# Kernel tuning notes

Measured on AMD Instinct MI355X. Metric: run time of the kernel, lower is better.

Reference implementation:

```python
import jax, jax.numpy as jnp
import numpy as np

EPS = 1e-06
SIGMA_C = 2.0


def setup_inputs() -> dict:
    key = jax.random.key(0)
    k1, k2 = jax.random.split(key)
    B, L, D, T = 16, 512, 256, 2048
    text = jax.random.normal(k1, (B, L, D), dtype=jnp.float32)
    durs = jax.random.randint(k2, (B, L), 0, 8, dtype=jnp.int64)
    return {"text": text, "durs": durs, "total_time": T}


def reference(text, durs, total_time):
    # text: [B, L, D], durs: [B, L] int, total_time: static python int T
    d = durs.astype(jnp.float32)
    # NOTE: faithful to original: mean = durs/2 + cumsum(durs) (cumsum includes current dur)
    mean = d / 2.0 + jnp.cumsum(d, axis=-1)            # [B, L]
    sigma = d / SIGMA_C + EPS                          # [B, L]
    t = jnp.arange(total_time, dtype=jnp.float32) + 0.5  # [T]
    # Normal pdf evaluated at t: exp(log_prob) = exp(-0.5 z^2) / (sigma * sqrt(2 pi))
    z = (t[None, :, None] - mean[:, None, :]) / sigma[:, None, :]  # [B, T, L]
    inv_norm = 1.0 / (sigma[:, None, :] * jnp.sqrt(2.0 * jnp.pi))
    probs = jnp.exp(-0.5 * z * z) * inv_norm           # [B, T, L]
    probs = probs / (probs.sum(-1, keepdims=True) + EPS)
    return jnp.einsum("btl,bld->btd", probs, text)     # [B, T, D]
```

## Files before the change

### kernel.cpp

```cpp
#include <hip/hip_runtime.h>
#include <math.h>

#define L 512
#define LPAD 544
#define NTHREADS 256
#define BLOCK_TT 32
#define ZWIN 9.0f
#define NXCD 8

typedef __attribute__((ext_vector_type(8))) short bf16x8;
typedef __attribute__((ext_vector_type(4))) float f32x4;

static constexpr float EPS = 1e-6f;
static constexpr float INV_SQRT_2PI = 0.39894228040143267794f;

union BFrag { unsigned int u[4]; bf16x8 h; };

__global__ __launch_bounds__(NTHREADS, 4) void ge_mfma(
    const int*   __restrict__ durs,
    const float* __restrict__ text,
    float*       __restrict__ out,
    int B, int T, int tilesPerB, int nwg)
{
    __shared__ float2 s_mi[LPAD];

    const int tid  = threadIdx.x;
    const int lane = tid & 63;
    const int wid  = tid >> 6;
    const int g    = lane >> 4;
    const int mrow = lane & 15;

    const int orig = blockIdx.x;
    const int wg   = (nwg % NXCD == 0) ? (orig & (NXCD - 1)) * (nwg / NXCD) + (orig >> 3)
                                       : orig;
    const int b      = wg / tilesPerB;
    const int tbase0 = (wg % tilesPerB) * BLOCK_TT;

    const int r0 = lane << 3;
    const int4 da = ((const int4*)(durs + (size_t)b * L + r0))[0];
    const int4 db = ((const int4*)(durs + (size_t)b * L + r0))[1];
    int dv[8] = {da.x, da.y, da.z, da.w, db.x, db.y, db.z, db.w};
    int cs[8];
    int run = 0;
    #pragma unroll
    for (int j = 0; j < 8; ++j) { run += dv[j]; cs[j] = run; }
    int v = run;
    #pragma unroll
    for (int off = 1; off < 64; off <<= 1) {
        int n = __shfl_up(v, off, 64);
        if (lane >= off) v += n;
    }
    const int excl = v - run;

    const float tlo = (float)tbase0 + 0.5f;
    const float thi = (float)tbase0 + (float)BLOCK_TT - 0.5f;
    int mn = L, mx = -1;
    #pragma unroll
    for (int j = 0; j < 8; ++j) {
        const float d  = (float)dv[j];
        const float m  = (float)(cs[j] + excl) + 0.5f * d;
        const float sg = 0.5f * d + EPS;
        s_mi[r0 + j] = make_float2(m, 1.0f / sg);
        const float r = ZWIN * sg;
        if (dv[j] >= 1 && m + r >= tlo && m - r <= thi) {
            mn = min(mn, r0 + j);
            mx = max(mx, r0 + j);
        }
    }
    if (lane < LPAD - L) s_mi[L + lane] = make_float2(0.f, 0.f);
    #pragma unroll
    for (int off = 32; off > 0; off >>= 1) {
        mn = min(mn, __shfl_xor(mn, off, 64));
        mx = max(mx, __shfl_xor(mx, off, 64));
    }
    asm volatile("s_waitcnt lgkmcnt(0)" ::: "memory");
    __builtin_amdgcn_sched_barrier(0);

    f32x4 a00 = {0,0,0,0}, a01 = {0,0,0,0}, a02 = {0,0,0,0}, a03 = {0,0,0,0};
    f32x4 a10 = {0,0,0,0}, a11 = {0,0,0,0}, a12 = {0,0,0,0}, a13 = {0,0,0,0};
    float psum0 = 0.f, psum1 = 0.f;
    const float tf0 = (float)(tbase0 + mrow) + 0.5f;
    const float tf1 = tf0 + 16.f;
    const float* tbp = text + (size_t)b * L * 256 + (wid << 6) + mrow;

    for (int kb = (mn & ~7); kb <= mx; kb += 32) {
        const int k0 = kb + (g << 3);

        BFrag B0, B1, B2, B3;
        #pragma unroll
        for (int jp = 0; jp < 4; ++jp) {
            const int ka = min(k0 + 2 * jp,     L - 1);
            const int kc = min(k0 + 2 * jp + 1, L - 1);
            const float* ra = tbp + (size_t)ka * 256;
            const float* rc = tbp + (size_t)kc * 256;
            const float b0 = ra[0], b1 = ra[16], b2 = ra[32], b3 = ra[48];
            const float c0 = rc[0], c1 = rc[16], c2 = rc[32], c3 = rc[48];
            asm("v_cvt_pk_bf16_f32 %0, %1, %2" : "=v"(B0.u[jp]) : "v"(b0), "v"(c0));
            asm("v_cvt_pk_bf16_f32 %0, %1, %2" : "=v"(B1.u[jp]) : "v"(b1), "v"(c1));
            asm("v_cvt_pk_bf16_f32 %0, %1, %2" : "=v"(B2.u[jp]) : "v"(b2), "v"(c2));
            asm("v_cvt_pk_bf16_f32 %0, %1, %2" : "=v"(B3.u[jp]) : "v"(b3), "v"(c3));
        }

        BFrag A0, A1;
        #pragma unroll
        for (int jp = 0; jp < 4; ++jp) {
            const int ka = k0 + 2 * jp;
            const int kc = ka + 1;
            const float2 mia = s_mi[ka];
            const float2 mic = s_mi[kc];
            const float ca = mia.y * INV_SQRT_2PI;
            const float cc = mic.y * INV_SQRT_2PI;
            const float u0a = (tf0 - mia.x) * mia.y;
            const float u0c = (tf0 - mic.x) * mic.y;
            const float u1a = (tf1 - mia.x) * mia.y;
            const float u1c = (tf1 - mic.x) * mic.y;
            const float p0a = __expf(-0.5f * u0a * u0a) * ca;
            const float p0c = __expf(-0.5f * u0c * u0c) * cc;
            const float p1a = __expf(-0.5f * u1a * u1a) * ca;
            const float p1c = __expf(-0.5f * u1c * u1c) * cc;
            psum0 += p0a + p0c;
            psum1 += p1a + p1c;
            asm("v_cvt_pk_bf16_f32 %0, %1, %2" : "=v"(A0.u[jp]) : "v"(p0a), "v"(p0c));
            asm("v_cvt_pk_bf16_f32 %0, %1, %2" : "=v"(A1.u[jp]) : "v"(p1a), "v"(p1c));
        }

        a00 = __builtin_amdgcn_mfma_f32_16x16x32_bf16(A0.h, B0.h, a00, 0, 0, 0);
        a01 = __builtin_amdgcn_mfma_f32_16x16x32_bf16(A0.h, B1.h, a01, 0, 0, 0);
        a02 = __builtin_amdgcn_mfma_f32_16x16x32_bf16(A0.h, B2.h, a02, 0, 0, 0);
        a03 = __builtin_amdgcn_mfma_f32_16x16x32_bf16(A0.h, B3.h, a03, 0, 0, 0);
        a10 = __builtin_amdgcn_mfma_f32_16x16x32_bf16(A1.h, B0.h, a10, 0, 0, 0);
        a11 = __builtin_amdgcn_mfma_f32_16x16x32_bf16(A1.h, B1.h, a11, 0, 0, 0);
        a12 = __builtin_amdgcn_mfma_f32_16x16x32_bf16(A1.h, B2.h, a12, 0, 0, 0);
        a13 = __builtin_amdgcn_mfma_f32_16x16x32_bf16(A1.h, B3.h, a13, 0, 0, 0);
    }

    const int trow = g << 2;
    #pragma unroll
    for (int half = 0; half < 2; ++half) {
        float ps = half ? psum1 : psum0;
        ps += __shfl_xor(ps, 16, 64);
        ps += __shfl_xor(ps, 32, 64);
        const float rn = 1.0f / (ps + EPS);

        const float rr0 = __shfl(rn, trow + 0, 64);
        const float rr1 = __shfl(rn, trow + 1, 64);
        const float rr2 = __shfl(rn, trow + 2, 64);
        const float rr3 = __shfl(rn, trow + 3, 64);

        const f32x4 c0 = half ? a10 : a00;
        const f32x4 c1 = half ? a11 : a01;
        const f32x4 c2 = half ? a12 : a02;
        const f32x4 c3 = half ? a13 : a03;

        const int t0 = tbase0 + (half << 4);
        float* ob = out + ((size_t)b * T + t0 + trow) * 256 + (wid << 6) + mrow;
        if (t0 + trow + 3 < T) {
            __builtin_nontemporal_store(c0[0] * rr0, ob + 0*256 +  0);
            __builtin_nontemporal_store(c0[1] * rr1, ob + 1*256 +  0);
            __builtin_nontemporal_store(c0[2] * rr2, ob + 2*256 +  0);
            __builtin_nontemporal_store(c0[3] * rr3, ob + 3*256 +  0);
            __builtin_nontemporal_store(c1[0] * rr0, ob + 0*256 + 16);
            __builtin_nontemporal_store(c1[1] * rr1, ob + 1*256 + 16);
            __builtin_nontemporal_store(c1[2] * rr2, ob + 2*256 + 16);
            __builtin_nontemporal_store(c1[3] * rr3, ob + 3*256 + 16);
            __builtin_nontemporal_store(c2[0] * rr0, ob + 0*256 + 32);
            __builtin_nontemporal_store(c2[1] * rr1, ob + 1*256 + 32);
            __builtin_nontemporal_store(c2[2] * rr2, ob + 2*256 + 32);
            __builtin_nontemporal_store(c2[3] * rr3, ob + 3*256 + 32);
            __builtin_nontemporal_store(c3[0] * rr0, ob + 0*256 + 48);
            __builtin_nontemporal_store(c3[1] * rr1, ob + 1*256 + 48);
            __builtin_nontemporal_store(c3[2] * rr2, ob + 2*256 + 48);
            __builtin_nontemporal_store(c3[3] * rr3, ob + 3*256 + 48);
        }
    }
}

extern "C" void kernel_launch(void* const* d_in, const int* in_sizes, int n_in,
                              void* d_out, int out_size, void* d_ws, size_t ws_size,
                              hipStream_t stream) {
    const int*   durs = (const int*)d_in[1];
    const float* text = (const float*)d_in[0];
    float*       out  = (float*)d_out;

    const int BL = in_sizes[1];
    const int D  = in_sizes[0] / BL;
    const int B  = BL / L;
    const int T  = out_size / (B * D);
    const int tilesPerB = (T + BLOCK_TT - 1) / BLOCK_TT;
    const int nwg = B * tilesPerB;

    ge_mfma<<<dim3(nwg), dim3(NTHREADS), 0, stream>>>(durs, text, out, B, T, tilesPerB, nwg);
}
```

Before: 14.57 us.

## Compute Gaussian weights once per block in LDS instead of per wave

Each of the four waves previously recomputed the same 32x32 tile of Gaussian probabilities. Now only waves 0 and 1 compute them, each handling one 16-row half, and write bf16 fragments and row sums to shared memory, which all waves read before the MFMAs. This removes redundant exp work but adds a __syncthreads per k-step, LDS traffic, and leaves two waves idle during the weight computation. Row sums are accumulated in shared memory and read in the epilogue, and a double-buffered fragment index is used.

```diff
diff --git a/kernel.cpp b/kernel.cpp
--- a/kernel.cpp
+++ b/kernel.cpp
@@ -14,7 +14,7 @@
 static constexpr float EPS = 1e-6f;
 static constexpr float INV_SQRT_2PI = 0.39894228040143267794f;
 
-union BFrag { unsigned int u[4]; bf16x8 h; };
+union BFrag { unsigned int u[4]; uint4 q; bf16x8 h; };
 
 __global__ __launch_bounds__(NTHREADS, 4) void ge_mfma(
     const int*   __restrict__ durs,
@@ -23,6 +23,8 @@
     int B, int T, int tilesPerB, int nwg)
 {
     __shared__ float2 s_mi[LPAD];
+    __shared__ uint4  s_af[2][2][64];
+    __shared__ float  s_ps[2][16];
 
     const int tid  = threadIdx.x;
     const int lane = tid & 63;
@@ -67,21 +69,19 @@
             mx = max(mx, r0 + j);
         }
     }
-    if (lane < LPAD - L) s_mi[L + lane] = make_float2(0.f, 0.f);
+    if (tid < LPAD - L) s_mi[L + tid] = make_float2(0.f, 0.f);
+    if (tid < 32) s_ps[tid >> 4][tid & 15] = 0.f;
     #pragma unroll
     for (int off = 32; off > 0; off >>= 1) {
         mn = min(mn, __shfl_xor(mn, off, 64));
         mx = max(mx, __shfl_xor(mx, off, 64));
     }
-    asm volatile("s_waitcnt lgkmcnt(0)" ::: "memory");
-    __builtin_amdgcn_sched_barrier(0);
+    __syncthreads();
 
     f32x4 a00 = {0,0,0,0}, a01 = {0,0,0,0}, a02 = {0,0,0,0}, a03 = {0,0,0,0};
     f32x4 a10 = {0,0,0,0}, a11 = {0,0,0,0}, a12 = {0,0,0,0}, a13 = {0,0,0,0};
-    float psum0 = 0.f, psum1 = 0.f;
-    const float tf0 = (float)(tbase0 + mrow) + 0.5f;
-    const float tf1 = tf0 + 16.f;
     const float* tbp = text + (size_t)b * L * 256 + (wid << 6) + mrow;
+    int p = 0;
 
     for (int kb = (mn & ~7); kb <= mx; kb += 32) {
         const int k0 = kb + (g << 3);
@@ -101,28 +101,48 @@
             asm("v_cvt_pk_bf16_f32 %0, %1, %2" : "=v"(B3.u[jp]) : "v"(b3), "v"(c3));
         }
 
+        if (wid < 2) {
+            const float tf = (float)(tbase0 + (wid << 4) + mrow) + 0.5f;
+            float part = 0.f;
+            unsigned int u0, u1, u2, u3;
+            {
+                const float2 mia = s_mi[k0 + 0], mic = s_mi[k0 + 1];
+                const float pa = __expf(-0.5f * ((tf - mia.x) * mia.y) * ((tf - mia.x) * mia.y)) * mia.y * INV_SQRT_2PI;
+                const float pc = __expf(-0.5f * ((tf - mic.x) * mic.y) * ((tf - mic.x) * mic.y)) * mic.y * INV_SQRT_2PI;
+                part += pa + pc;
+                asm("v_cvt_pk_bf16_f32 %0, %1, %2" : "=v"(u0) : "v"(pa), "v"(pc));
+            }
+            {
+                const float2 mia = s_mi[k0 + 2], mic = s_mi[k0 + 3];
+                const float pa = __expf(-0.5f * ((tf - mia.x) * mia.y) * ((tf - mia.x) * mia.y)) * mia.y * INV_SQRT_2PI;
+                const float pc = __expf(-0.5f * ((tf - mic.x) * mic.y) * ((tf - mic.x) * mic.y)) * mic.y * INV_SQRT_2PI;
+                part += pa + pc;
+                asm("v_cvt_pk_bf16_f32 %0, %1, %2" : "=v"(u1) : "v"(pa), "v"(pc));
+            }
+            {
+                const float2 mia = s_mi[k0 + 4], mic = s_mi[k0 + 5];
+                const float pa = __expf(-0.5f * ((tf - mia.x) * mia.y) * ((tf - mia.x) * mia.y)) * mia.y * INV_SQRT_2PI;
+                const float pc = __expf(-0.5f * ((tf - mic.x) * mic.y) * ((tf - mic.x) * mic.y)) * mic.y * INV_SQRT_2PI;
+                part += pa + pc;
+                asm("v_cvt_pk_bf16_f32 %0, %1, %2" : "=v"(u2) : "v"(pa), "v"(pc));
+            }
+            {
+                const float2 mia = s_mi[k0 + 6], mic = s_mi[k0 + 7];
+                const float pa = __expf(-0.5f * ((tf - mia.x) * mia.y) * ((tf - mia.x) * mia.y)) * mia.y * INV_SQRT_2PI;
+                const float pc = __expf(-0.5f * ((tf - mic.x) * mic.y) * ((tf - mic.x) * mic.y)) * mic.y * INV_SQRT_2PI;
+                part += pa + pc;
+                asm("v_cvt_pk_bf16_f32 %0, %1, %2" : "=v"(u3) : "v"(pa), "v"(pc));
+            }
+            part += __shfl_xor(part, 16, 64);
+            part += __shfl_xor(part, 32, 64);
+            if (lane < 16) s_ps[wid][lane] += part;
+            s_af[p][wid][lane] = make_uint4(u0, u1, u2, u3);
+        }
+        __syncthreads();
+
         BFrag A0, A1;
-        #pragma unroll
-        for (int jp = 0; jp < 4; ++jp) {
-            const int ka = k0 + 2 * jp;
-            const int kc = ka + 1;
-            const float2 mia = s_mi[ka];
-            const float2 mic = s_mi[kc];
-            const float ca = mia.y * INV_SQRT_2PI;
-            const float cc = mic.y * INV_SQRT_2PI;
-            const float u0a = (tf0 - mia.x) * mia.y;
-            const float u0c = (tf0 - mic.x) * mic.y;
-            const float u1a = (tf1 - mia.x) * mia.y;
-            const float u1c = (tf1 - mic.x) * mic.y;
-            const float p0a = __expf(-0.5f * u0a * u0a) * ca;
-            const float p0c = __expf(-0.5f * u0c * u0c) * cc;
-            const float p1a = __expf(-0.5f * u1a * u1a) * ca;
-            const float p1c = __expf(-0.5f * u1c * u1c) * cc;
-            psum0 += p0a + p0c;
-            psum1 += p1a + p1c;
-            asm("v_cvt_pk_bf16_f32 %0, %1, %2" : "=v"(A0.u[jp]) : "v"(p0a), "v"(p0c));
-            asm("v_cvt_pk_bf16_f32 %0, %1, %2" : "=v"(A1.u[jp]) : "v"(p1a), "v"(p1c));
-        }
+        A0.q = s_af[p][0][lane];
+        A1.q = s_af[p][1][lane];
 
         a00 = __builtin_amdgcn_mfma_f32_16x16x32_bf16(A0.h, B0.h, a00, 0, 0, 0);
         a01 = __builtin_amdgcn_mfma_f32_16x16x32_bf16(A0.h, B1.h, a01, 0, 0, 0);
@@ -132,20 +152,16 @@
         a11 = __builtin_amdgcn_mfma_f32_16x16x32_bf16(A1.h, B1.h, a11, 0, 0, 0);
         a12 = __builtin_amdgcn_mfma_f32_16x16x32_bf16(A1.h, B2.h, a12, 0, 0, 0);
         a13 = __builtin_amdgcn_mfma_f32_16x16x32_bf16(A1.h, B3.h, a13, 0, 0, 0);
+        p ^= 1;
     }
 
     const int trow = g << 2;
     #pragma unroll
     for (int half = 0; half < 2; ++half) {
-        float ps = half ? psum1 : psum0;
-        ps += __shfl_xor(ps, 16, 64);
-        ps += __shfl_xor(ps, 32, 64);
-        const float rn = 1.0f / (ps + EPS);
-
-        const float rr0 = __shfl(rn, trow + 0, 64);
-        const float rr1 = __shfl(rn, trow + 1, 64);
-        const float rr2 = __shfl(rn, trow + 2, 64);
-        const float rr3 = __shfl(rn, trow + 3, 64);
+        const float rr0 = 1.0f / (s_ps[half][trow + 0] + EPS);
+        const float rr1 = 1.0f / (s_ps[half][trow + 1] + EPS);
+        const float rr2 = 1.0f / (s_ps[half][trow + 2] + EPS);
+        const float rr3 = 1.0f / (s_ps[half][trow + 3] + EPS);
 
         const f32x4 c0 = half ? a10 : a00;
         const f32x4 c1 = half ? a11 : a01;
```

Measured after the change: 15.48 us. 1.06x slower.
